# Optimization experiments

Measured on AMD Instinct MI355X. Metric: run time of the kernel, lower is better.

Reference implementation:

```python
import jax, jax.numpy as jnp
import numpy as np

EMBED_DIM = 96
OUT_DIM = 192
HEADS = 2
HEAD_DIM = OUT_DIM // HEADS  # 96
STRIDE_Q = (1, 2, 2)
STRIDE_KV = (1, 8, 8)
SCALE = 1.0 / float(np.sqrt(HEAD_DIM))


def layer_norm(x, g, b, eps=1e-5):
    m = jnp.mean(x, -1, keepdims=True)
    v = jnp.mean(jnp.square(x - m), -1, keepdims=True)
    return (x - m) * jax.lax.rsqrt(v + eps) * g + b


def pool(x, thw, conv_w, g, b, stride):
    # x: [B, heads, N, d] with cls token at position 0; depthwise conv3d pool + LayerNorm(d)
    B, nh, N, d = x.shape
    T, H, W = thw
    cls_tok, rest = x[:, :, :1], x[:, :, 1:]
    rest = rest.transpose(0, 1, 3, 2).reshape(B * nh, d, T, H, W)
    rest = jax.lax.conv_general_dilated(
        rest, conv_w, stride, [(1, 1), (1, 1), (1, 1)],
        dimension_numbers=('NCDHW', 'OIDHW', 'NCDHW'), feature_group_count=d)
    T2, H2, W2 = rest.shape[2], rest.shape[3], rest.shape[4]
    rest = rest.reshape(B, nh, d, -1).transpose(0, 1, 3, 2)
    x = jnp.concatenate([cls_tok, rest], axis=2)
    return layer_norm(x, g, b), (T2, H2, W2)


def rel_idx(q_n, k_n):
    # decomposed relative-distance indices with q/k resolution ratio scaling
    q_r = max(k_n / q_n, 1.0)
    k_r = max(q_n / k_n, 1.0)
    d = (jnp.arange(q_n, dtype=jnp.float32)[:, None] * q_r
         - jnp.arange(k_n, dtype=jnp.float32)[None, :] * k_r + (k_n - 1) * k_r)
    return d.astype(jnp.int32)


def add_rel_pos(attn, q, q_thw, k_thw, rph, rpw, rpt):
    qt, qh, qw = q_thw
    kt, kh, kw = k_thw
    Rh = rph[rel_idx(qh, kh)]  # [qh, kh, d]
    Rw = rpw[rel_idx(qw, kw)]  # [qw, kw, d]
    Rt = rpt[rel_idx(qt, kt)]  # [qt, kt, d]
    B, nh, qN, d = q.shape
    r_q = q[:, :, 1:].reshape(B, nh, qt, qh, qw, d)
    rel_h = jnp.einsum('bythwc,hkc->bythwk', r_q, Rh)  # k = kh
    rel_w = jnp.einsum('bythwc,wkc->bythwk', r_q, Rw)  # k = kw
    rel_t = jnp.einsum('bythwc,tkc->bythwk', r_q, Rt)  # k = kt
    rel = (rel_t[..., :, None, None] + rel_h[..., None, :, None]
           + rel_w[..., None, None, :]).reshape(B, nh, qt * qh * qw, kt * kh * kw)
    return attn.at[:, :, 1:, 1:].add(rel)


def _forward(x, qkv_w, qkv_b, proj_w, proj_b, pq_w, nq_g, nq_b, pk_w, nk_g, nk_b,
             pv_w, nv_g, nv_b, rel_pos_h, rel_pos_w, rel_pos_t, thw):
    B, N, C = x.shape
    qkv = (x @ qkv_w.T + qkv_b).reshape(B, N, 3, HEADS, HEAD_DIM).transpose(2, 0, 3, 1, 4)
    q, k, v = qkv[0], qkv[1], qkv[2]  # each [B, heads, N, head_dim]
    k, k_thw = pool(k, thw, pk_w, nk_g, nk_b, STRIDE_KV)
    v, _ = pool(v, thw, pv_w, nv_g, nv_b, STRIDE_KV)
    q, q_thw = pool(q, thw, pq_w, nq_g, nq_b, STRIDE_Q)
    attn = jnp.einsum('bhqd,bhkd->bhqk', q * SCALE, k)
    attn = add_rel_pos(attn, q, q_thw, k_thw, rel_pos_h, rel_pos_w, rel_pos_t)
    attn = jax.nn.softmax(attn, axis=-1)
    out = jnp.einsum('bhqk,bhkd->bhqd', attn, v) + q  # residual_pool, with cls embed
    out = out.transpose(0, 2, 1, 3).reshape(B, -1, OUT_DIM)
    return out @ proj_w.T + proj_b


def setup_inputs() -> dict:
    key = jax.random.key(0)
    ks = jax.random.split(key, 10)
    T, H, W = 8, 56, 56
    N = 1 + T * H * W  # 25089
    B = 4
    std = 0.02
    return {
        'x': jax.random.normal(ks[0], (B, N, EMBED_DIM), jnp.float32),
        'qkv_w': jax.random.normal(ks[1], (3 * OUT_DIM, EMBED_DIM), jnp.float32) * std,
        'qkv_b': jnp.zeros((3 * OUT_DIM,), jnp.float32),
        'proj_w': jax.random.normal(ks[2], (OUT_DIM, OUT_DIM), jnp.float32) * std,
        'proj_b': jnp.zeros((OUT_DIM,), jnp.float32),
        'pq_w': jax.random.normal(ks[3], (HEAD_DIM, 1, 3, 3, 3), jnp.float32) * std,
        'nq_g': jnp.ones((HEAD_DIM,), jnp.float32),
        'nq_b': jnp.zeros((HEAD_DIM,), jnp.float32),
        'pk_w': jax.random.normal(ks[4], (HEAD_DIM, 1, 3, 3, 3), jnp.float32) * std,
        'nk_g': jnp.ones((HEAD_DIM,), jnp.float32),
        'nk_b': jnp.zeros((HEAD_DIM,), jnp.float32),
        'pv_w': jax.random.normal(ks[5], (HEAD_DIM, 1, 3, 3, 3), jnp.float32) * std,
        'nv_g': jnp.ones((HEAD_DIM,), jnp.float32),
        'nv_b': jnp.zeros((HEAD_DIM,), jnp.float32),
        'rel_pos_h': jax.random.normal(ks[6], (55, HEAD_DIM), jnp.float32) * std,
        'rel_pos_w': jax.random.normal(ks[7], (55, HEAD_DIM), jnp.float32) * std,
        'rel_pos_t': jax.random.normal(ks[8], (15, HEAD_DIM), jnp.float32) * std,
        'thw_t': 8, 'thw_h': 56, 'thw_w': 56,
    }


def reference(x, qkv_w, qkv_b, proj_w, proj_b, pq_w, nq_g, nq_b, pk_w, nk_g, nk_b,
              pv_w, nv_g, nv_b, rel_pos_h, rel_pos_w, rel_pos_t, thw_t, thw_h, thw_w):
    thw = (int(thw_t), int(thw_h), int(thw_w))
    return _forward(x, qkv_w, qkv_b, proj_w, proj_b, pq_w, nq_g, nq_b, pk_w, nk_g, nk_b,
                    pv_w, nv_g, nv_b, rel_pos_h, rel_pos_w, rel_pos_t, thw)
```

## Files before the change

kernel.cpp:

```cpp
#include <hip/hip_runtime.h>
#include <hip/hip_bf16.h>

typedef short short8 __attribute__((ext_vector_type(8)));
typedef float floatx4 __attribute__((ext_vector_type(4)));
typedef float floatx4v __attribute__((ext_vector_type(4)));

#define SCALE_F 0.10206207261596575f
#define TOKSTRIDE 401424

static __device__ __forceinline__ float b2f(unsigned short u){
  unsigned int v = ((unsigned int)u) << 16; float f;
  __builtin_memcpy(&f, &v, 4); return f;
}
static __device__ __forceinline__ unsigned short f2b(float f){
  __hip_bfloat16 h = __float2bfloat16(f);
  unsigned short u; __builtin_memcpy(&u, &h, 2); return u;
}
static __device__ __forceinline__ int map20(int i){
  return (i < 2) ? i : 7 + ((i-2)/3)*8 + ((i-2)%3);
}

struct ConvDesc {
  const void* src[17];
  long long off[17];
  int count[17];
};

__global__ __launch_bounds__(256) void k_convert(ConvDesc d, unsigned short* dst_base,
                                                 int* flagp, const unsigned int* xprobe)
{
  __shared__ int sflag;
  if (threadIdx.x < 64){
    unsigned int w = xprobe[1024 + threadIdx.x];
    int e = (w >> 7) & 0xFF;
    int pl = (e >= 90 && e <= 140) ? 1 : 0;
    unsigned long long m = __ballot(pl);
    if (threadIdx.x == 0){
      sflag = (__popcll(m) < 40) ? 1 : 0;
      if (blockIdx.x == 0 && blockIdx.y == 0) *flagp = sflag;
    }
  }
  __syncthreads();
  const int flag = sflag;
  const int t = blockIdx.y + 1;
  const int cnt = d.count[t];
  unsigned short* dst = dst_base + d.off[t];
  const float* sf = (const float*)d.src[t];
  const unsigned short* su = (const unsigned short*)d.src[t];
  for (int i = blockIdx.x*blockDim.x + threadIdx.x; i < cnt; i += gridDim.x*blockDim.x){
    dst[i] = flag ? f2b(sf[i]) : su[i];
  }
}

static __device__ __forceinline__ void load_x_frag(
    const void* xr_, int flag, size_t elem_off, short8& a0, short8& a1, short8& a2)
{
  if (flag){
    const float* xr = (const float*)xr_ + elem_off;
    floatx4v f0 = *(const floatx4v*)(xr),      f1 = *(const floatx4v*)(xr+4);
    floatx4v f2 = *(const floatx4v*)(xr+32),   f3 = *(const floatx4v*)(xr+36);
    floatx4v f4 = *(const floatx4v*)(xr+64),   f5 = *(const floatx4v*)(xr+68);
    #pragma unroll
    for (int j = 0; j < 4; ++j){
      a0[j] = (short)f2b(f0[j]); a0[j+4] = (short)f2b(f1[j]);
      a1[j] = (short)f2b(f2[j]); a1[j+4] = (short)f2b(f3[j]);
      a2[j] = (short)f2b(f4[j]); a2[j+4] = (short)f2b(f5[j]);
    }
  } else {
    const unsigned short* xr = (const unsigned short*)xr_ + elem_off;
    a0 = *(const short8*)(xr);
    a1 = *(const short8*)(xr + 32);
    a2 = *(const short8*)(xr + 64);
  }
}

__global__ __launch_bounds__(256) void k_qkv(
    const void* __restrict__ x, const unsigned short* __restrict__ w,
    const unsigned short* __restrict__ bias, unsigned short* __restrict__ qr,
    unsigned short* __restrict__ kc, unsigned short* __restrict__ vc,
    unsigned short* __restrict__ kcls, unsigned short* __restrict__ vcls,
    const int* __restrict__ flagp)
{
  const int flag = *flagp;
  const int lane = threadIdx.x & 63;
  const int wv = threadIdx.x >> 6;
  const int kq = (lane >> 4) * 8;
  const int quad = lane >> 4;
  const int col_l = lane & 15;

  if (blockIdx.x < 1569){
    const int m_base = blockIdx.x * 64 + wv * 16;
    int ma = m_base + col_l; if (ma > 100355) ma = 100355;
    short8 a0, a1, a2;
    load_x_frag(x, flag, (size_t)ma*96 + kq, a0, a1, a2);

    int bbase[4], ntok[4], mrow[4];
    #pragma unroll
    for (int r = 0; r < 4; ++r){
      int m = m_base + quad*4 + r;
      mrow[r] = m;
      int bb = m / 25089;
      ntok[r] = m - bb*25089;
      bbase[r] = bb*2;
    }

    #pragma unroll
    for (int ct = 0; ct < 12; ++ct){
      int col = ct*16 + col_l;
      const unsigned short* wrow = w + col*96 + kq;
      short8 b0 = *(const short8*)(wrow);
      short8 b1 = *(const short8*)(wrow + 32);
      short8 b2 = *(const short8*)(wrow + 64);
      float bv = b2f(bias[col]);
      floatx4 acc = {0.f,0.f,0.f,0.f};
      acc = __builtin_amdgcn_mfma_f32_16x16x32_bf16(a0, b0, acc, 0,0,0);
      acc = __builtin_amdgcn_mfma_f32_16x16x32_bf16(a1, b1, acc, 0,0,0);
      acc = __builtin_amdgcn_mfma_f32_16x16x32_bf16(a2, b2, acc, 0,0,0);
      const int head = ct / 6;
      const int dt6  = ct % 6;
      #pragma unroll
      for (int r = 0; r < 4; ++r){
        if (mrow[r] < 100356)
          qr[(size_t)((bbase[r]+head)*6 + dt6)*TOKSTRIDE + (size_t)ntok[r]*16 + col_l]
            = f2b(acc[r] + bv);
      }
    }
  } else {
    const int id = blockIdx.x - 1569;
    const int isv = id / 201;
    const int bx = id - isv*201;
    const int rbase = bx * 64 + wv * 16;

    int rhoA = rbase + col_l; if (rhoA > 12803) rhoA = 12803;
    int bA, nA;
    if (rhoA < 4){ bA = rhoA; nA = 0; }
    else {
      int rp = rhoA - 4;
      bA = rp / 3200; int rem = rp - bA*3200;
      int t = rem / 400; int s = rem - t*400;
      int ry = s / 20, rx = s - ry*20;
      nA = 1 + (t*56 + map20(ry))*56 + map20(rx);
    }
    short8 a0, a1, a2;
    load_x_frag(x, flag, ((size_t)bA*25089 + nA)*96 + kq, a0, a1, a2);

    int isCls[4], bI[4], baseI[4], valid[4];
    #pragma unroll
    for (int r = 0; r < 4; ++r){
      int rho = rbase + quad*4 + r;
      valid[r] = (rho < 12804);
      if (rho > 12803) rho = 12803;
      if (rho < 4){ isCls[r] = 1; bI[r] = rho; baseI[r] = 0; }
      else {
        int rp = rho - 4;
        int b = rp / 3200; int rem = rp - b*3200;
        int t = rem / 400; int s = rem - t*400;
        int ry = s / 20, rx = s - ry*20;
        isCls[r] = 0; bI[r] = b;
        baseI[r] = (((b*8 + t)*20 + ry)*20 + rx)*192;
      }
    }

    unsigned short* buf  = isv ? vc : kc;
    unsigned short* bufc = isv ? vcls : kcls;
    #pragma unroll
    for (int ct = 0; ct < 12; ++ct){
      const int col = 192 + (isv*12 + ct)*16 + col_l;
      const unsigned short* wrow = w + col*96 + kq;
      short8 b0 = *(const short8*)(wrow);
      short8 b1 = *(const short8*)(wrow + 32);
      short8 b2 = *(const short8*)(wrow + 64);
      float bv = b2f(bias[col]);
      floatx4 acc = {0.f,0.f,0.f,0.f};
      acc = __builtin_amdgcn_mfma_f32_16x16x32_bf16(a0, b0, acc, 0,0,0);
      acc = __builtin_amdgcn_mfma_f32_16x16x32_bf16(a1, b1, acc, 0,0,0);
      acc = __builtin_amdgcn_mfma_f32_16x16x32_bf16(a2, b2, acc, 0,0,0);
      const int head = ct / 6;
      const int dstat = (ct % 6) * 16;
      #pragma unroll
      for (int r = 0; r < 4; ++r){
        if (valid[r]){
          float o = acc[r] + bv;
          if (isCls[r]) bufc[(bI[r]*2 + head)*96 + dstat + col_l] = f2b(o);
          else          buf[baseI[r] + head*96 + dstat + col_l]   = f2b(o);
        }
      }
    }
  }
}

__global__ __launch_bounds__(384) void k_pool(
    const unsigned short* __restrict__ qr, const unsigned short* __restrict__ cwq,
    const unsigned short* __restrict__ gq, const unsigned short* __restrict__ btaq,
    unsigned short* __restrict__ qp,
    const unsigned short* __restrict__ kc, const unsigned short* __restrict__ vc,
    const unsigned short* __restrict__ kcls, const unsigned short* __restrict__ vcls,
    const unsigned short* __restrict__ cwk, const unsigned short* __restrict__ gk, const unsigned short* __restrict__ bk,
    const unsigned short* __restrict__ cwv, const unsigned short* __restrict__ gv, const unsigned short* __restrict__ bv,
    unsigned short* __restrict__ kp, unsigned short* __restrict__ vt)
{
  const int tid = threadIdx.x;
  if (blockIdx.x < 1792){
    __shared__ float wlds[27*96];
    __shared__ float gls[96], bls[96];
    __shared__ float ls1[29*12], ls2[29*12];
    __shared__ float lmean[29], linvs[29];

    const int bid = blockIdx.x;
    const int y  = bid % 28;
    const int t  = (bid / 28) % 8;
    const int bh = bid / 224;
    const bool has_cls = (y == 0 && t == 0);

    for (int idx = tid; idx < 27*96; idx += 384){
      int tap = idx / 96, d = idx - tap*96;
      wlds[idx] = b2f(cwq[d*27 + tap]);
    }
    for (int idx = tid; idx < 96; idx += 384){
      gls[idx] = b2f(gq[idx]); bls[idx] = b2f(btaq[idx]);
    }
    __syncthreads();

    const int x = tid / 12, dg = tid - x*12;
    const unsigned short* rowb = qr + (size_t)(bh*6 + (dg >> 1))*TOKSTRIDE + (dg & 1)*8;
    float val[8] = {0,0,0,0,0,0,0,0};

    if (x < 28){
      #pragma unroll
      for (int dt = 0; dt < 3; ++dt){
        int tt = t + dt - 1; if (tt < 0 || tt >= 8) continue;
        #pragma unroll
        for (int dy = 0; dy < 3; ++dy){
          int yy = 2*y + dy - 1; if (yy < 0 || yy >= 56) continue;
          #pragma unroll
          for (int dx = 0; dx < 3; ++dx){
            int xv = 2*x + dx - 1; if (xv < 0 || xv >= 56) continue;
            const int tap = (dt*3+dy)*3+dx;
            short8 v = *(const short8*)(rowb + (size_t)(1 + (tt*56 + yy)*56 + xv)*16);
            const float* wr = wlds + tap*96 + dg*8;
            #pragma unroll
            for (int j = 0; j < 8; ++j) val[j] += b2f((unsigned short)v[j]) * wr[j];
          }
        }
      }
      float s1 = 0.f, s2 = 0.f;
      #pragma unroll
      for (int j = 0; j < 8; ++j){ s1 += val[j]; s2 += val[j]*val[j]; }
      ls1[x*12+dg] = s1; ls2[x*12+dg] = s2;
    } else if (has_cls && tid >= 348 && tid < 360){
      int cdg = tid - 348;
      const unsigned short* rowc = qr + (size_t)(bh*6 + (cdg >> 1))*TOKSTRIDE + (cdg & 1)*8;
      short8 v = *(const short8*)(rowc);
      float s1 = 0.f, s2 = 0.f;
      #pragma unroll
      for (int j = 0; j < 8; ++j){ val[j] = b2f((unsigned short)v[j]); s1 += val[j]; s2 += val[j]*val[j]; }
      ls1[28*12+cdg] = s1; ls2[28*12+cdg] = s2;
    }
    __syncthreads();

    if (tid < 28 || (tid == 28 && has_cls)){
      float s1 = 0.f, s2 = 0.f;
      #pragma unroll
      for (int k = 0; k < 12; ++k){ s1 += ls1[tid*12+k]; s2 += ls2[tid*12+k]; }
      float mean = s1 * (1.f/96.f);
      float var  = s2 * (1.f/96.f) - mean*mean;
      lmean[tid] = mean; linvs[tid] = rsqrtf(var + 1e-5f);
    }
    __syncthreads();

    if (x < 28){
      float mean = lmean[x], inv = linvs[x];
      int tok = 1 + (t*28 + y)*28 + x;
      short8 o;
      #pragma unroll
      for (int j = 0; j < 8; ++j)
        o[j] = (short)f2b((val[j] - mean)*inv*gls[dg*8+j] + bls[dg*8+j]);
      *(short8*)(qp + ((size_t)bh*6273 + tok)*96 + dg*8) = o;
    } else if (has_cls && tid >= 348 && tid < 360){
      int cdg = tid - 348;
      float mean = lmean[28], inv = linvs[28];
      short8 o;
      #pragma unroll
      for (int j = 0; j < 8; ++j)
        o[j] = (short)f2b((val[j] - mean)*inv*gls[cdg*8+j] + bls[cdg*8+j]);
      *(short8*)(qp + (size_t)bh*6273*96 + cdg*8) = o;
    }
  } else {
    __shared__ float r1[3][128], r2s[3][128];
    const int unit = tid >> 7;
    const int d = tid & 127;
    const int u = (blockIdx.x - 1792)*3 + unit;
    const bool live = (u < 6656);
    int isv = 0, bh = 0, key = 0;
    if (live){
      isv = u / 3328; int rem = u - isv*3328;
      bh = rem / 416; key = rem - bh*416;
    }
    const bool pad = (key >= 393);
    const int b = bh >> 1, head = bh & 1;
    const unsigned short* buf  = isv ? vc : kc;
    const unsigned short* bufc = isv ? vcls : kcls;
    const unsigned short* cw = (isv == 0) ? cwk : cwv;
    const unsigned short* g  = (isv == 0) ? gk : gv;
    const unsigned short* bt = (isv == 0) ? bk : bv;

    float val = 0.f;
    if (live && !pad && d < 96){
      if (key == 0) val = b2f(bufc[bh*96 + d]);
      else {
        int s = key - 1; int t = s / 49; int r2 = s - t*49; int y = r2 / 7; int xx = r2 - y*7;
        const unsigned short* wr = cw + d*27;
        float sum = 0.f;
        #pragma unroll
        for (int dt = 0; dt < 3; ++dt){
          int tt = t + dt - 1; if (tt < 0 || tt >= 8) continue;
          #pragma unroll
          for (int dy = 0; dy < 3; ++dy){
            if (y == 0 && dy == 0) continue;
            int ry = (y == 0) ? (dy - 1) : 2 + 3*(y-1) + dy;
            #pragma unroll
            for (int dx = 0; dx < 3; ++dx){
              if (xx == 0 && dx == 0) continue;
              int rx = (xx == 0) ? (dx - 1) : 2 + 3*(xx-1) + dx;
              sum += b2f(buf[(((b*8 + tt)*20 + ry)*20 + rx)*192 + head*96 + d]) * b2f(wr[(dt*3+dy)*3+dx]);
            }
          }
        }
        val = sum;
      }
    }
    r1[unit][d]  = (d < 96) ? val : 0.f;
    r2s[unit][d] = (d < 96) ? val*val : 0.f;
    __syncthreads();
    for (int off = 64; off > 0; off >>= 1){
      if (d < off){ r1[unit][d] += r1[unit][d+off]; r2s[unit][d] += r2s[unit][d+off]; }
      __syncthreads();
    }
    if (live && d < 96){
      float mean = r1[unit][0] * (1.f/96.f);
      float var  = r2s[unit][0] * (1.f/96.f) - mean*mean;
      float inv = rsqrtf(var + 1e-5f);
      float o = pad ? 0.f : (val - mean)*inv*b2f(g[d]) + b2f(bt[d]);
      if (isv == 0) kp[((size_t)bh*416 + key)*96 + d] = f2b(o);
      else          vt[((size_t)bh*96 + d)*416 + key] = f2b(o);
    }
  }
}

#define PSTR 424
__global__ __launch_bounds__(256, 3) void k_attn(
    const unsigned short* __restrict__ qp, const unsigned short* __restrict__ kp,
    const unsigned short* __restrict__ vt,
    const unsigned short* __restrict__ rph, const unsigned short* __restrict__ rpw,
    const unsigned short* __restrict__ rpt,
    unsigned short* __restrict__ ao)
{
  __shared__ unsigned short P[32*PSTR];
  __shared__ __align__(16) float rel[24*36 + 4];
  __shared__ float mx_sh[4][32], sum_sh[4][32];

  const int bh = blockIdx.y;
  const int bb = bh >> 1, head = bh & 1;
  const int tid = threadIdx.x;
  const int lane = tid & 63;
  const int wv = tid >> 6;
  const int q0 = blockIdx.x * 32;

  const unsigned short* qbase = qp + (size_t)bh*6273*96;
  const unsigned short* kbase = kp + (size_t)bh*416*96;
  const unsigned short* vbase = vt + (size_t)bh*96*416;

  const int col = lane & 15;
  const int quad = lane >> 4;
  const int kq = quad * 8;

  short8 aF[2][3];
  #pragma unroll
  for (int tl = 0; tl < 2; ++tl){
    int qa = q0 + tl*16 + col; if (qa > 6272) qa = 6272;
    const unsigned short* qrow = qbase + (size_t)qa*96 + kq;
    aF[tl][0] = *(const short8*)(qrow);
    aF[tl][1] = *(const short8*)(qrow + 32);
    aF[tl][2] = *(const short8*)(qrow + 64);
  }

  int yq[2][4], xq[2][4], tq[2][4], livx[2][4], liv[2][4];
  #pragma unroll
  for (int tl = 0; tl < 2; ++tl)
  #pragma unroll
  for (int r = 0; r < 4; ++r){
    int gq = q0 + tl*16 + quad*4 + r;
    liv[tl][r]  = (gq >= 1);
    livx[tl][r] = (gq >= 1 && gq <= 6272);
    int s = (gq >= 1) ? gq - 1 : 0;
    tq[tl][r] = s / 784; int r2 = s - tq[tl][r]*784; yq[tl][r] = r2 / 28; xq[tl][r] = r2 - yq[tl][r]*28;
  }

  #pragma unroll
  for (int j = 0; j < 2; ++j){
    const int c = (wv*2 + j)*16 + col;
    const unsigned short* rrow;
    if (c < 55)       rrow = rph + (size_t)c*96;
    else if (c < 110) rrow = rpw + (size_t)(c-55)*96;
    else { int ci = c-110; if (ci > 14) ci = 14; rrow = rpt + (size_t)ci*96; }
    rrow += kq;
    short8 b0 = *(const short8*)(rrow);
    short8 b1 = *(const short8*)(rrow + 32);
    short8 b2 = *(const short8*)(rrow + 64);
    #pragma unroll
    for (int tl = 0; tl < 2; ++tl){
      floatx4 rc = {0.f,0.f,0.f,0.f};
      rc = __builtin_amdgcn_mfma_f32_16x16x32_bf16(aF[tl][0], b0, rc, 0,0,0);
      rc = __builtin_amdgcn_mfma_f32_16x16x32_bf16(aF[tl][1], b1, rc, 0,0,0);
      rc = __builtin_amdgcn_mfma_f32_16x16x32_bf16(aF[tl][2], b2, rc, 0,0,0);
      #pragma unroll
      for (int r = 0; r < 4; ++r){
        if (!livx[tl][r]) continue;
        const int m = tl*16 + quad*4 + r;
        if (c < 55){
          int u = yq[tl][r] + 24 - c;
          if (u >= 0 && u <= 24 && (u & 3) == 0) rel[(u >> 2)*36 + m] = rc[r];
        } else if (c < 110){
          int u = xq[tl][r] + 24 - (c - 55);
          if (u >= 0 && u <= 24 && (u & 3) == 0) rel[(8 + (u >> 2))*36 + m] = rc[r];
        } else if (c < 125){
          int u = tq[tl][r] + 7 - (c - 110);
          if (u >= 0 && u <= 7) rel[(16 + u)*36 + m] = rc[r];
        }
      }
    }
  }
  __syncthreads();

  floatx4 acc[2][7];
  float mx[2][4] = {{-1e30f,-1e30f,-1e30f,-1e30f},{-1e30f,-1e30f,-1e30f,-1e30f}};
  #pragma unroll
  for (int i = 0; i < 7; ++i){
    int t = wv*7 + i; if (t > 25) t = 25;
    const unsigned short* krow = kbase + (size_t)(t*16 + col)*96 + kq;
    short8 b0 = *(const short8*)(krow);
    short8 b1 = *(const short8*)(krow + 32);
    short8 b2 = *(const short8*)(krow + 64);
    const int key = t*16 + col;
    const bool validk = (key < 393);
    int kt = 0, ky = 0, kx = 0;
    if (key >= 1 && validk){
      int ks = key - 1; kt = ks / 49; int krm = ks - kt*49; ky = krm / 7; kx = krm - ky*7;
    }
    floatx4v rh0 = *(const floatx4v*)(rel + ky*36 + quad*4);
    floatx4v rh1 = *(const floatx4v*)(rel + ky*36 + 16 + quad*4);
    floatx4v rw0 = *(const floatx4v*)(rel + (8 + kx)*36 + quad*4);
    floatx4v rw1 = *(const floatx4v*)(rel + (8 + kx)*36 + 16 + quad*4);
    floatx4v rt0 = *(const floatx4v*)(rel + (16 + kt)*36 + quad*4);
    floatx4v rt1 = *(const floatx4v*)(rel + (16 + kt)*36 + 16 + quad*4);
    #pragma unroll
    for (int tl = 0; tl < 2; ++tl){
      floatx4 a = {0.f,0.f,0.f,0.f};
      a = __builtin_amdgcn_mfma_f32_16x16x32_bf16(aF[tl][0], b0, a, 0,0,0);
      a = __builtin_amdgcn_mfma_f32_16x16x32_bf16(aF[tl][1], b1, a, 0,0,0);
      a = __builtin_amdgcn_mfma_f32_16x16x32_bf16(aF[tl][2], b2, a, 0,0,0);
      #pragma unroll
      for (int r = 0; r < 4; ++r){
        float s;
        if (!validk) s = -1e30f;
        else {
          s = a[r] * SCALE_F;
          if (key >= 1 && liv[tl][r]){
            float rhv = tl ? rh1[r] : rh0[r];
            float rwv = tl ? rw1[r] : rw0[r];
            float rtv = tl ? rt1[r] : rt0[r];
            s += rhv + rwv + rtv;
          }
        }
        a[r] = s;
        mx[tl][r] = fmaxf(mx[tl][r], s);
      }
      acc[tl][i] = a;
    }
  }
  #pragma unroll
  for (int tl = 0; tl < 2; ++tl)
  #pragma unroll
  for (int r = 0; r < 4; ++r){
    #pragma unroll
    for (int o = 1; o < 16; o <<= 1) mx[tl][r] = fmaxf(mx[tl][r], __shfl_xor(mx[tl][r], o, 64));
  }
  if (col == 0){
    #pragma unroll
    for (int tl = 0; tl < 2; ++tl)
    #pragma unroll
    for (int r = 0; r < 4; ++r) mx_sh[wv][tl*16 + quad*4 + r] = mx[tl][r];
  }
  __syncthreads();

  float M[2][4];
  #pragma unroll
  for (int tl = 0; tl < 2; ++tl)
  #pragma unroll
  for (int r = 0; r < 4; ++r){
    const int m = tl*16 + quad*4 + r;
    float m01 = fmaxf(mx_sh[0][m], mx_sh[1][m]);
    float m23 = fmaxf(mx_sh[2][m], mx_sh[3][m]);
    M[tl][r] = fmaxf(m01, m23);
  }
  float sum[2][4] = {{0.f,0.f,0.f,0.f},{0.f,0.f,0.f,0.f}};
  #pragma unroll
  for (int i = 0; i < 7; ++i){
    #pragma unroll
    for (int tl = 0; tl < 2; ++tl)
    #pragma unroll
    for (int r = 0; r < 4; ++r){
      float e = __expf(acc[tl][i][r] - M[tl][r]);
      acc[tl][i][r] = e; sum[tl][r] += e;
    }
  }
  #pragma unroll
  for (int tl = 0; tl < 2; ++tl)
  #pragma unroll
  for (int r = 0; r < 4; ++r){
    #pragma unroll
    for (int o = 1; o < 16; o <<= 1) sum[tl][r] += __shfl_xor(sum[tl][r], o, 64);
  }
  if (col == 0){
    #pragma unroll
    for (int tl = 0; tl < 2; ++tl)
    #pragma unroll
    for (int r = 0; r < 4; ++r) sum_sh[wv][tl*16 + quad*4 + r] = sum[tl][r];
  }
  #pragma unroll
  for (int i = 0; i < 7; ++i){
    int t = wv*7 + i; if (t > 25) t = 25;
    #pragma unroll
    for (int tl = 0; tl < 2; ++tl)
    #pragma unroll
    for (int r = 0; r < 4; ++r)
      P[(tl*16 + quad*4 + r)*PSTR + t*16 + col] = f2b(acc[tl][i][r]);
  }
  __syncthreads();

  const int tlw = wv >> 1;
  float linv4[4];
  #pragma unroll
  for (int r = 0; r < 4; ++r){
    const int m = tlw*16 + quad*4 + r;
    linv4[r] = 1.f / (sum_sh[0][m] + sum_sh[1][m] + sum_sh[2][m] + sum_sh[3][m]);
  }

  short8 pf[13];
  #pragma unroll
  for (int s = 0; s < 13; ++s)
    pf[s] = *(const short8*)(P + (tlw*16 + col)*PSTR + s*32 + kq);

  #pragma unroll
  for (int j = 0; j < 3; ++j){
    const int slot = (wv & 1)*3 + j;
    const int dd = slot*16 + col;
    const unsigned short* vrow = vbase + (size_t)dd*416 + kq;
    floatx4 o = {0.f,0.f,0.f,0.f};
    #pragma unroll
    for (int s = 0; s < 13; ++s){
      short8 vf = *(const short8*)(vrow + s*32);
      o = __builtin_amdgcn_mfma_f32_16x16x32_bf16(pf[s], vf, o, 0,0,0);
    }
    #pragma unroll
    for (int r = 0; r < 4; ++r){
      int gq = q0 + tlw*16 + quad*4 + r;
      if (gq <= 6272){
        float val = o[r] * linv4[r] + b2f(qbase[(size_t)gq*96 + dd]);
        ao[((size_t)bb*6273 + gq)*192 + head*96 + dd] = f2b(val);
      }
    }
  }
}

__global__ __launch_bounds__(256) void k_proj(
    const unsigned short* __restrict__ ao, const unsigned short* __restrict__ w,
    const unsigned short* __restrict__ bias, void* __restrict__ out, const int* __restrict__ flagp)
{
  const int flag = *flagp;
  const int lane = threadIdx.x & 63;
  const int wv = threadIdx.x >> 6;
  const int c = blockIdx.y*64 + wv*16 + (lane & 15);
  const int kq = (lane >> 4) * 8;
  short8 bfr[6];
  const unsigned short* wrow = w + c*192 + kq;
  #pragma unroll
  for (int s = 0; s < 6; ++s) bfr[s] = *(const short8*)(wrow + 32*s);
  float bv = b2f(bias[c]);
  const int m_base = blockIdx.x * 64;
  for (int i = 0; i < 4; ++i){
    int mt = m_base + i*16;
    int ma = mt + (lane & 15); if (ma > 25091) ma = 25091;
    const unsigned short* arow = ao + (size_t)ma*192 + kq;
    floatx4 acc = {0.f,0.f,0.f,0.f};
    #pragma unroll
    for (int s = 0; s < 6; ++s){
      short8 a = *(const short8*)(arow + 32*s);
      acc = __builtin_amdgcn_mfma_f32_16x16x32_bf16(a, bfr[s], acc, 0,0,0);
    }
    #pragma unroll
    for (int r = 0; r < 4; ++r){
      int m = mt + (lane >> 4)*4 + r;
      if (m < 25092){
        float o = acc[r] + bv;
        if (flag) ((float*)out)[(size_t)m*192 + c] = o;
        else      ((unsigned short*)out)[(size_t)m*192 + c] = f2b(o);
      }
    }
  }
}

extern "C" void kernel_launch(void* const* d_in, const int* in_sizes, int n_in,
                              void* d_out, int out_size, void* d_ws, size_t ws_size,
                              hipStream_t stream)
{
  char* p = (char*)d_ws;
  int* flagp = (int*)p; p += 16;
  unsigned short* conv = (unsigned short*)p;

  ConvDesc desc;
  long long cum = 0;
  for (int i = 0; i < 17; ++i){
    desc.src[i] = d_in[i];
    desc.off[i] = cum;
    desc.count[i] = in_sizes[i];
    cum += in_sizes[i];
  }
  p += (size_t)cum * 2;

  unsigned short* q_raw  = (unsigned short*)p; p += (size_t)19268352*2;
  unsigned short* kc     = (unsigned short*)p; p += (size_t)2457600*2;
  unsigned short* vc     = (unsigned short*)p; p += (size_t)2457600*2;
  unsigned short* kcls   = (unsigned short*)p; p += (size_t)768*2;
  unsigned short* vcls   = (unsigned short*)p; p += (size_t)768*2;
  unsigned short* q_pool = (unsigned short*)p; p += (size_t)4817664*2;
  unsigned short* kp_buf = (unsigned short*)p; p += (size_t)319488*2;
  unsigned short* v_t    = (unsigned short*)p; p += (size_t)319488*2;
  unsigned short* a_out  = q_raw;

  const unsigned short* cqkv_w = conv + desc.off[1];
  const unsigned short* cqkv_b = conv + desc.off[2];
  const unsigned short* cproj_w= conv + desc.off[3];
  const unsigned short* cproj_b= conv + desc.off[4];
  const unsigned short* cpq_w  = conv + desc.off[5];
  const unsigned short* cnq_g  = conv + desc.off[6];
  const unsigned short* cnq_b  = conv + desc.off[7];
  const unsigned short* cpk_w  = conv + desc.off[8];
  const unsigned short* cnk_g  = conv + desc.off[9];
  const unsigned short* cnk_b  = conv + desc.off[10];
  const unsigned short* cpv_w  = conv + desc.off[11];
  const unsigned short* cnv_g  = conv + desc.off[12];
  const unsigned short* cnv_b  = conv + desc.off[13];
  const unsigned short* crph   = conv + desc.off[14];
  const unsigned short* crpw   = conv + desc.off[15];
  const unsigned short* crpt   = conv + desc.off[16];

  k_convert<<<dim3(16, 16), 256, 0, stream>>>(desc, conv, flagp, (const unsigned int*)d_in[0]);
  k_qkv  <<<dim3(1971), 256, 0, stream>>>(d_in[0], cqkv_w, cqkv_b, q_raw, kc, vc, kcls, vcls, flagp);
  k_pool <<<dim3(4011), 384, 0, stream>>>(q_raw, cpq_w, cnq_g, cnq_b, q_pool,
                                          kc, vc, kcls, vcls,
                                          cpk_w, cnk_g, cnk_b, cpv_w, cnv_g, cnv_b, kp_buf, v_t);
  k_attn <<<dim3(197, 8), 256, 0, stream>>>(q_pool, kp_buf, v_t, crph, crpw, crpt, a_out);
  k_proj <<<dim3(393, 3), 256, 0, stream>>>(a_out, cproj_w, cproj_b, d_out, flagp);
}
```

Before: 264.1 us.

## Split pool kernel and stage Q conv input rows through padded LDS

The fused pooling kernel is split into separate Q-pool and KV-pool kernels. The Q pooling kernel now loads three input rows per temporal tap into shared memory, split by x-parity so strided neighbours are contiguous. The 3x3 spatial taps then read from LDS instead of issuing nine separate global loads per thread. This cuts redundant global traffic and uses a smaller per-kernel LDS footprint. In exchange it adds an extra kernel launch, more barriers and larger shared memory for the Q blocks.

```diff
diff --git a/kernel.cpp b/kernel.cpp
--- a/kernel.cpp
+++ b/kernel.cpp
@@ -189,10 +189,126 @@
   }
 }
 
-__global__ __launch_bounds__(384) void k_pool(
+#define QP_PAD 104
+__global__ __launch_bounds__(384) void k_qpool(
     const unsigned short* __restrict__ qr, const unsigned short* __restrict__ cwq,
     const unsigned short* __restrict__ gq, const unsigned short* __restrict__ btaq,
-    unsigned short* __restrict__ qp,
+    unsigned short* __restrict__ qp)
+{
+  __shared__ float wlds[27*96];
+  __shared__ float gls[96], bls[96];
+  __shared__ float ls1[29*12], ls2[29*12];
+  __shared__ float lmean[29], linvs[29];
+  __shared__ __align__(16) unsigned short stg[3*2*29*QP_PAD];
+
+  const int tid = threadIdx.x;
+  const int bid = blockIdx.x;
+  const int y  = bid % 28;
+  const int t  = (bid / 28) % 8;
+  const int bh = bid / 224;
+  const bool has_cls = (y == 0 && t == 0);
+
+  for (int idx = tid; idx < 27*96; idx += 384){
+    int tap = idx / 96, d = idx - tap*96;
+    wlds[idx] = b2f(cwq[d*27 + tap]);
+  }
+  for (int idx = tid; idx < 96; idx += 384){
+    gls[idx] = b2f(gq[idx]); bls[idx] = b2f(btaq[idx]);
+  }
+  {
+    short8 z = {0,0,0,0,0,0,0,0};
+    for (int idx = tid; idx < 39; idx += 384){
+      int yy = idx / 13, o = idx - yy*13;
+      *(short8*)(stg + (yy*2)*29*QP_PAD + o*8) = z;
+    }
+  }
+
+  const int x = tid / 12, dg = tid - x*12;
+  float val[8] = {0,0,0,0,0,0,0,0};
+  __syncthreads();
+
+  for (int dt = 0; dt < 3; ++dt){
+    const int tt = t + dt - 1;
+    const bool tok_valid = (tt >= 0 && tt < 8);
+    if (tok_valid){
+      short8 z = {0,0,0,0,0,0,0,0};
+      for (int i = tid; i < 2016; i += 384){
+        int chunk = i / 112, o = i - chunk*112;
+        int yy = chunk / 6, pl = chunk - yy*6;
+        int xv = o >> 1, half = o & 1;
+        int yg = 2*y + yy - 1;
+        short8 v = z;
+        if (yg >= 0)
+          v = *(const short8*)(qr + (size_t)(bh*6+pl)*TOKSTRIDE
+                               + (size_t)(1 + (tt*56+yg)*56 + xv)*16 + half*8);
+        int s = xv + 1;
+        *(short8*)(stg + ((yy*2 + (s&1))*29 + (s>>1))*QP_PAD + pl*16 + half*8) = v;
+      }
+    }
+    __syncthreads();
+    if (tok_valid && x < 28){
+      #pragma unroll
+      for (int dy = 0; dy < 3; ++dy){
+        #pragma unroll
+        for (int dx = 0; dx < 3; ++dx){
+          const unsigned short* sp = stg
+            + ((dy*2 + (dx&1))*29 + x + (dx>>1))*QP_PAD + dg*8;
+          short8 v = *(const short8*)(sp);
+          const float* wr = wlds + ((dt*3+dy)*3+dx)*96 + dg*8;
+          #pragma unroll
+          for (int j = 0; j < 8; ++j) val[j] += b2f((unsigned short)v[j]) * wr[j];
+        }
+      }
+    }
+    __syncthreads();
+  }
+
+  if (x < 28){
+    float s1 = 0.f, s2 = 0.f;
+    #pragma unroll
+    for (int j = 0; j < 8; ++j){ s1 += val[j]; s2 += val[j]*val[j]; }
+    ls1[x*12+dg] = s1; ls2[x*12+dg] = s2;
+  } else if (has_cls && tid >= 348 && tid < 360){
+    int cdg = tid - 348;
+    const unsigned short* rowc = qr + (size_t)(bh*6 + (cdg >> 1))*TOKSTRIDE + (cdg & 1)*8;
+    short8 v = *(const short8*)(rowc);
+    float s1 = 0.f, s2 = 0.f;
+    #pragma unroll
+    for (int j = 0; j < 8; ++j){ val[j] = b2f((unsigned short)v[j]); s1 += val[j]; s2 += val[j]*val[j]; }
+    ls1[28*12+cdg] = s1; ls2[28*12+cdg] = s2;
+  }
+  __syncthreads();
+
+  if (tid < 28 || (tid == 28 && has_cls)){
+    float s1 = 0.f, s2 = 0.f;
+    #pragma unroll
+    for (int k = 0; k < 12; ++k){ s1 += ls1[tid*12+k]; s2 += ls2[tid*12+k]; }
+    float mean = s1 * (1.f/96.f);
+    float var  = s2 * (1.f/96.f) - mean*mean;
+    lmean[tid] = mean; linvs[tid] = rsqrtf(var + 1e-5f);
+  }
+  __syncthreads();
+
+  if (x < 28){
+    float mean = lmean[x], inv = linvs[x];
+    int tok = 1 + (t*28 + y)*28 + x;
+    short8 o;
+    #pragma unroll
+    for (int j = 0; j < 8; ++j)
+      o[j] = (short)f2b((val[j] - mean)*inv*gls[dg*8+j] + bls[dg*8+j]);
+    *(short8*)(qp + ((size_t)bh*6273 + tok)*96 + dg*8) = o;
+  } else if (has_cls && tid >= 348 && tid < 360){
+    int cdg = tid - 348;
+    float mean = lmean[28], inv = linvs[28];
+    short8 o;
+    #pragma unroll
+    for (int j = 0; j < 8; ++j)
+      o[j] = (short)f2b((val[j] - mean)*inv*gls[cdg*8+j] + bls[cdg*8+j]);
+    *(short8*)(qp + (size_t)bh*6273*96 + cdg*8) = o;
+  }
+}
+
+__global__ __launch_bounds__(384) void k_kvpool(
     const unsigned short* __restrict__ kc, const unsigned short* __restrict__ vc,
     const unsigned short* __restrict__ kcls, const unsigned short* __restrict__ vcls,
     const unsigned short* __restrict__ cwk, const unsigned short* __restrict__ gk, const unsigned short* __restrict__ bk,
@@ -200,150 +316,63 @@
     unsigned short* __restrict__ kp, unsigned short* __restrict__ vt)
 {
   const int tid = threadIdx.x;
-  if (blockIdx.x < 1792){
-    __shared__ float wlds[27*96];
-    __shared__ float gls[96], bls[96];
-    __shared__ float ls1[29*12], ls2[29*12];
-    __shared__ float lmean[29], linvs[29];
-
-    const int bid = blockIdx.x;
-    const int y  = bid % 28;
-    const int t  = (bid / 28) % 8;
-    const int bh = bid / 224;
-    const bool has_cls = (y == 0 && t == 0);
-
-    for (int idx = tid; idx < 27*96; idx += 384){
-      int tap = idx / 96, d = idx - tap*96;
-      wlds[idx] = b2f(cwq[d*27 + tap]);
-    }
-    for (int idx = tid; idx < 96; idx += 384){
-      gls[idx] = b2f(gq[idx]); bls[idx] = b2f(btaq[idx]);
-    }
-    __syncthreads();
-
-    const int x = tid / 12, dg = tid - x*12;
-    const unsigned short* rowb = qr + (size_t)(bh*6 + (dg >> 1))*TOKSTRIDE + (dg & 1)*8;
-    float val[8] = {0,0,0,0,0,0,0,0};
-
-    if (x < 28){
+  __shared__ float r1[3][128], r2s[3][128];
+  const int unit = tid >> 7;
+  const int d = tid & 127;
+  const int u = blockIdx.x*3 + unit;
+  const bool live = (u < 6656);
+  int isv = 0, bh = 0, key = 0;
+  if (live){
+    isv = u / 3328; int rem = u - isv*3328;
+    bh = rem / 416; key = rem - bh*416;
+  }
+  const bool pad = (key >= 393);
+  const int b = bh >> 1, head = bh & 1;
+  const unsigned short* buf  = isv ? vc : kc;
+  const unsigned short* bufc = isv ? vcls : kcls;
+  const unsigned short* cw = (isv == 0) ? cwk : cwv;
+  const unsigned short* g  = (isv == 0) ? gk : gv;
+  const unsigned short* bt = (isv == 0) ? bk : bv;
+
+  float val = 0.f;
+  if (live && !pad && d < 96){
+    if (key == 0) val = b2f(bufc[bh*96 + d]);
+    else {
+      int s = key - 1; int t = s / 49; int r2 = s - t*49; int y = r2 / 7; int xx = r2 - y*7;
+      const unsigned short* wr = cw + d*27;
+      float sum = 0.f;
       #pragma unroll
       for (int dt = 0; dt < 3; ++dt){
         int tt = t + dt - 1; if (tt < 0 || tt >= 8) continue;
         #pragma unroll
         for (int dy = 0; dy < 3; ++dy){
-          int yy = 2*y + dy - 1; if (yy < 0 || yy >= 56) continue;
+          if (y == 0 && dy == 0) continue;
+          int ry = (y == 0) ? (dy - 1) : 2 + 3*(y-1) + dy;
           #pragma unroll
           for (int dx = 0; dx < 3; ++dx){
-            int xv = 2*x + dx - 1; if (xv < 0 || xv >= 56) continue;
-            const int tap = (dt*3+dy)*3+dx;
-            short8 v = *(const short8*)(rowb + (size_t)(1 + (tt*56 + yy)*56 + xv)*16);
-            const float* wr = wlds + tap*96 + dg*8;
-            #pragma unroll
-            for (int j = 0; j < 8; ++j) val[j] += b2f((unsigned short)v[j]) * wr[j];
+            if (xx == 0 && dx == 0) continue;
+            int rx = (xx == 0) ? (dx - 1) : 2 + 3*(xx-1) + dx;
+            sum += b2f(buf[(((b*8 + tt)*20 + ry)*20 + rx)*192 + head*96 + d]) * b2f(wr[(dt*3+dy)*3+dx]);
           }
         }
       }
-      float s1 = 0.f, s2 = 0.f;
-      #pragma unroll
-      for (int j = 0; j < 8; ++j){ s1 += val[j]; s2 += val[j]*val[j]; }
-      ls1[x*12+dg] = s1; ls2[x*12+dg] = s2;
-    } else if (has_cls && tid >= 348 && tid < 360){
-      int cdg = tid - 348;
-      const unsigned short* rowc = qr + (size_t)(bh*6 + (cdg >> 1))*TOKSTRIDE + (cdg & 1)*8;
-      short8 v = *(const short8*)(rowc);
-      float s1 = 0.f, s2 = 0.f;
-      #pragma unroll
-      for (int j = 0; j < 8; ++j){ val[j] = b2f((unsigned short)v[j]); s1 += val[j]; s2 += val[j]*val[j]; }
-      ls1[28*12+cdg] = s1; ls2[28*12+cdg] = s2;
-    }
+      val = sum;
+    }
+  }
+  r1[unit][d]  = (d < 96) ? val : 0.f;
+  r2s[unit][d] = (d < 96) ? val*val : 0.f;
+  __syncthreads();
+  for (int off = 64; off > 0; off >>= 1){
+    if (d < off){ r1[unit][d] += r1[unit][d+off]; r2s[unit][d] += r2s[unit][d+off]; }
     __syncthreads();
-
-    if (tid < 28 || (tid == 28 && has_cls)){
-      float s1 = 0.f, s2 = 0.f;
-      #pragma unroll
-      for (int k = 0; k < 12; ++k){ s1 += ls1[tid*12+k]; s2 += ls2[tid*12+k]; }
-      float mean = s1 * (1.f/96.f);
-      float var  = s2 * (1.f/96.f) - mean*mean;
-      lmean[tid] = mean; linvs[tid] = rsqrtf(var + 1e-5f);
-    }
-    __syncthreads();
-
-    if (x < 28){
-      float mean = lmean[x], inv = linvs[x];
-      int tok = 1 + (t*28 + y)*28 + x;
-      short8 o;
-      #pragma unroll
-      for (int j = 0; j < 8; ++j)
-        o[j] = (short)f2b((val[j] - mean)*inv*gls[dg*8+j] + bls[dg*8+j]);
-      *(short8*)(qp + ((size_t)bh*6273 + tok)*96 + dg*8) = o;
-    } else if (has_cls && tid >= 348 && tid < 360){
-      int cdg = tid - 348;
-      float mean = lmean[28], inv = linvs[28];
-      short8 o;
-      #pragma unroll
-      for (int j = 0; j < 8; ++j)
-        o[j] = (short)f2b((val[j] - mean)*inv*gls[cdg*8+j] + bls[cdg*8+j]);
-      *(short8*)(qp + (size_t)bh*6273*96 + cdg*8) = o;
-    }
-  } else {
-    __shared__ float r1[3][128], r2s[3][128];
-    const int unit = tid >> 7;
-    const int d = tid & 127;
-    const int u = (blockIdx.x - 1792)*3 + unit;
-    const bool live = (u < 6656);
-    int isv = 0, bh = 0, key = 0;
-    if (live){
-      isv = u / 3328; int rem = u - isv*3328;
-      bh = rem / 416; key = rem - bh*416;
-    }
-    const bool pad = (key >= 393);
-    const int b = bh >> 1, head = bh & 1;
-    const unsigned short* buf  = isv ? vc : kc;
-    const unsigned short* bufc = isv ? vcls : kcls;
-    const unsigned short* cw = (isv == 0) ? cwk : cwv;
-    const unsigned short* g  = (isv == 0) ? gk : gv;
-    const unsigned short* bt = (isv == 0) ? bk : bv;
-
-    float val = 0.f;
-    if (live && !pad && d < 96){
-      if (key == 0) val = b2f(bufc[bh*96 + d]);
-      else {
-        int s = key - 1; int t = s / 49; int r2 = s - t*49; int y = r2 / 7; int xx = r2 - y*7;
-        const unsigned short* wr = cw + d*27;
-        float sum = 0.f;
-        #pragma unroll
-        for (int dt = 0; dt < 3; ++dt){
-          int tt = t + dt - 1; if (tt < 0 || tt >= 8) continue;
-          #pragma unroll
-          for (int dy = 0; dy < 3; ++dy){
-            if (y == 0 && dy == 0) continue;
-            int ry = (y == 0) ? (dy - 1) : 2 + 3*(y-1) + dy;
-            #pragma unroll
-            for (int dx = 0; dx < 3; ++dx){
-              if (xx == 0 && dx == 0) continue;
-              int rx = (xx == 0) ? (dx - 1) : 2 + 3*(xx-1) + dx;
-              sum += b2f(buf[(((b*8 + tt)*20 + ry)*20 + rx)*192 + head*96 + d]) * b2f(wr[(dt*3+dy)*3+dx]);
-            }
-          }
-        }
-        val = sum;
-      }
-    }
-    r1[unit][d]  = (d < 96) ? val : 0.f;
-    r2s[unit][d] = (d < 96) ? val*val : 0.f;
-    __syncthreads();
-    for (int off = 64; off > 0; off >>= 1){
-      if (d < off){ r1[unit][d] += r1[unit][d+off]; r2s[unit][d] += r2s[unit][d+off]; }
-      __syncthreads();
-    }
-    if (live && d < 96){
-      float mean = r1[unit][0] * (1.f/96.f);
-      float var  = r2s[unit][0] * (1.f/96.f) - mean*mean;
-      float inv = rsqrtf(var + 1e-5f);
-      float o = pad ? 0.f : (val - mean)*inv*b2f(g[d]) + b2f(bt[d]);
-      if (isv == 0) kp[((size_t)bh*416 + key)*96 + d] = f2b(o);
-      else          vt[((size_t)bh*96 + d)*416 + key] = f2b(o);
-    }
+  }
+  if (live && d < 96){
+    float mean = r1[unit][0] * (1.f/96.f);
+    float var  = r2s[unit][0] * (1.f/96.f) - mean*mean;
+    float inv = rsqrtf(var + 1e-5f);
+    float o = pad ? 0.f : (val - mean)*inv*b2f(g[d]) + b2f(bt[d]);
+    if (isv == 0) kp[((size_t)bh*416 + key)*96 + d] = f2b(o);
+    else          vt[((size_t)bh*96 + d)*416 + key] = f2b(o);
   }
 }
 
@@ -656,10 +685,10 @@
   const unsigned short* crpt   = conv + desc.off[16];
 
   k_convert<<<dim3(16, 16), 256, 0, stream>>>(desc, conv, flagp, (const unsigned int*)d_in[0]);
-  k_qkv  <<<dim3(1971), 256, 0, stream>>>(d_in[0], cqkv_w, cqkv_b, q_raw, kc, vc, kcls, vcls, flagp);
-  k_pool <<<dim3(4011), 384, 0, stream>>>(q_raw, cpq_w, cnq_g, cnq_b, q_pool,
-                                          kc, vc, kcls, vcls,
-                                          cpk_w, cnk_g, cnk_b, cpv_w, cnv_g, cnv_b, kp_buf, v_t);
-  k_attn <<<dim3(197, 8), 256, 0, stream>>>(q_pool, kp_buf, v_t, crph, crpw, crpt, a_out);
-  k_proj <<<dim3(393, 3), 256, 0, stream>>>(a_out, cproj_w, cproj_b, d_out, flagp);
-}
+  k_qkv   <<<dim3(1971), 256, 0, stream>>>(d_in[0], cqkv_w, cqkv_b, q_raw, kc, vc, kcls, vcls, flagp);
+  k_qpool <<<dim3(1792), 384, 0, stream>>>(q_raw, cpq_w, cnq_g, cnq_b, q_pool);
+  k_kvpool<<<dim3(2219), 384, 0, stream>>>(kc, vc, kcls, vcls,
+                                           cpk_w, cnk_g, cnk_b, cpv_w, cnv_g, cnv_b, kp_buf, v_t);
+  k_attn  <<<dim3(197, 8), 256, 0, stream>>>(q_pool, kp_buf, v_t, crph, crpw, crpt, a_out);
+  k_proj  <<<dim3(393, 3), 256, 0, stream>>>(a_out, cproj_w, cproj_b, d_out, flagp);
+}
```

After: 290.9 us. 1.1x slower.

## Store Q projection token-major via LDS staging for coalesced 16-byte writes

Applied to the files above, without the earlier changes.

Changes the intermediate q buffer layout from a split-channel (6 planes of 16 dims) layout to a plain token-major [bh, token, 96] layout. The QKV kernel now stages the MFMA outputs in shared memory and writes them out as coalesced 16-byte vectors instead of scattered 2-byte stores. The pooling kernel reads the new layout with matching indexing. This adds an LDS tile and a barrier in the projection kernel, and the pooling reads now have a 192-byte token stride.

```diff
diff --git a/kernel.cpp b/kernel.cpp
--- a/kernel.cpp
+++ b/kernel.cpp
@@ -6,7 +6,6 @@
 typedef float floatx4v __attribute__((ext_vector_type(4)));
 
 #define SCALE_F 0.10206207261596575f
-#define TOKSTRIDE 401424
 
 static __device__ __forceinline__ float b2f(unsigned short u){
   unsigned int v = ((unsigned int)u) << 16; float f;
@@ -81,28 +80,21 @@
     unsigned short* __restrict__ kcls, unsigned short* __restrict__ vcls,
     const int* __restrict__ flagp)
 {
+  __shared__ __align__(16) unsigned short T[64*200];
   const int flag = *flagp;
-  const int lane = threadIdx.x & 63;
-  const int wv = threadIdx.x >> 6;
+  const int tid = threadIdx.x;
+  const int lane = tid & 63;
+  const int wv = tid >> 6;
   const int kq = (lane >> 4) * 8;
   const int quad = lane >> 4;
   const int col_l = lane & 15;
 
   if (blockIdx.x < 1569){
-    const int m_base = blockIdx.x * 64 + wv * 16;
-    int ma = m_base + col_l; if (ma > 100355) ma = 100355;
+    const int m_base = blockIdx.x * 64;
+    const int row_l = wv * 16;
+    int ma = m_base + row_l + col_l; if (ma > 100355) ma = 100355;
     short8 a0, a1, a2;
     load_x_frag(x, flag, (size_t)ma*96 + kq, a0, a1, a2);
-
-    int bbase[4], ntok[4], mrow[4];
-    #pragma unroll
-    for (int r = 0; r < 4; ++r){
-      int m = m_base + quad*4 + r;
-      mrow[r] = m;
-      int bb = m / 25089;
-      ntok[r] = m - bb*25089;
-      bbase[r] = bb*2;
-    }
 
     #pragma unroll
     for (int ct = 0; ct < 12; ++ct){
@@ -116,13 +108,26 @@
       acc = __builtin_amdgcn_mfma_f32_16x16x32_bf16(a0, b0, acc, 0,0,0);
       acc = __builtin_amdgcn_mfma_f32_16x16x32_bf16(a1, b1, acc, 0,0,0);
       acc = __builtin_amdgcn_mfma_f32_16x16x32_bf16(a2, b2, acc, 0,0,0);
-      const int head = ct / 6;
-      const int dt6  = ct % 6;
-      #pragma unroll
-      for (int r = 0; r < 4; ++r){
-        if (mrow[r] < 100356)
-          qr[(size_t)((bbase[r]+head)*6 + dt6)*TOKSTRIDE + (size_t)ntok[r]*16 + col_l]
-            = f2b(acc[r] + bv);
+      #pragma unroll
+      for (int r = 0; r < 4; ++r)
+        T[(row_l + quad*4 + r)*200 + ct*16 + col_l] = f2b(acc[r] + bv);
+    }
+    __syncthreads();
+
+    #pragma unroll
+    for (int k = 0; k < 6; ++k){
+      int c = tid + k*256;
+      int row = c / 24;
+      int off = c - row*24;
+      int m = m_base + row;
+      if (m < 100356){
+        int bb2 = m / 25089;
+        int ntok = m - bb2*25089;
+        int col8 = off*8;
+        int head = (col8 >= 96) ? 1 : 0;
+        int d = col8 - head*96;
+        short8 v = *(const short8*)(T + row*200 + col8);
+        *(short8*)(qr + ((size_t)(bb2*2 + head)*25089 + (size_t)ntok)*96 + d) = v;
       }
     }
   } else {
@@ -222,7 +227,7 @@
     __syncthreads();
 
     const int x = tid / 12, dg = tid - x*12;
-    const unsigned short* rowb = qr + (size_t)(bh*6 + (dg >> 1))*TOKSTRIDE + (dg & 1)*8;
+    const unsigned short* qbh = qr + (size_t)bh*25089*96;
     float val[8] = {0,0,0,0,0,0,0,0};
 
     if (x < 28){
@@ -236,7 +241,7 @@
           for (int dx = 0; dx < 3; ++dx){
             int xv = 2*x + dx - 1; if (xv < 0 || xv >= 56) continue;
             const int tap = (dt*3+dy)*3+dx;
-            short8 v = *(const short8*)(rowb + (size_t)(1 + (tt*56 + yy)*56 + xv)*16);
+            short8 v = *(const short8*)(qbh + (size_t)(1 + (tt*56 + yy)*56 + xv)*96 + dg*8);
             const float* wr = wlds + tap*96 + dg*8;
             #pragma unroll
             for (int j = 0; j < 8; ++j) val[j] += b2f((unsigned short)v[j]) * wr[j];
@@ -249,8 +254,7 @@
       ls1[x*12+dg] = s1; ls2[x*12+dg] = s2;
     } else if (has_cls && tid >= 348 && tid < 360){
       int cdg = tid - 348;
-      const unsigned short* rowc = qr + (size_t)(bh*6 + (cdg >> 1))*TOKSTRIDE + (cdg & 1)*8;
-      short8 v = *(const short8*)(rowc);
+      short8 v = *(const short8*)(qbh + cdg*8);
       float s1 = 0.f, s2 = 0.f;
       #pragma unroll
       for (int j = 0; j < 8; ++j){ val[j] = b2f((unsigned short)v[j]); s1 += val[j]; s2 += val[j]*val[j]; }
```

Result: no change. 260.0 us (-1.5%).
